# Optimization experiments

Measured on AMD Instinct MI355X. Metric: run time of the kernel, lower is better.

## Reference

```python
import jax, jax.numpy as jnp
import numpy as np


def _rgcn(x, src, dst, et, basis, comp, root, bias):
    # Basis-decomposed RGCNConv (PyG semantics): per-relation mean aggregation
    # over incoming edges + root transform + bias.
    N = x.shape[0]
    R = comp.shape[0]
    W = jnp.einsum('rb,bio->rio', comp, basis)          # [R, in, out]
    xr = jnp.einsum('ni,rio->rno', x, W)                 # [R, N, out]
    msg = xr[et, src]                                    # [E, out] gather per edge
    seg = dst * R + et                                   # (target, relation) segment id
    cnt = jax.ops.segment_sum(jnp.ones(et.shape, x.dtype), seg, num_segments=N * R)
    norm = 1.0 / jnp.maximum(cnt, 1.0)                   # mean per (dst, relation)
    msg = msg * norm[seg][:, None]
    agg = jax.ops.segment_sum(msg, dst, num_segments=N)  # scatter-add to targets
    return agg + x @ root + bias


def setup_inputs() -> dict:
    key = jax.random.key(0)
    ks = jax.random.split(key, 20)
    N, E, R, B, F, D, C, NB = 100000, 1600000, 5, 512, 4, 32, 5, 2
    s = 0.1
    inp = {
        'x': jax.random.normal(ks[0], (N, F), jnp.float32),
        'edge_index': jax.random.randint(ks[1], (2, E), 0, N, dtype=jnp.int32),
        'edge_type': jax.random.randint(ks[2], (E,), 0, R, dtype=jnp.int32),
        'start_nodes': jax.random.randint(ks[3], (B,), 0, N, dtype=jnp.int32),
        # layer 0: in=F, out=D
        'basis0': jax.random.normal(ks[4], (NB, F, D), jnp.float32) * s,
        'comp0': jax.random.normal(ks[5], (R, NB), jnp.float32) * s,
        'root0': jax.random.normal(ks[6], (F, D), jnp.float32) * s,
        'bias0': jax.random.normal(ks[7], (D,), jnp.float32) * s,
        # layers 1..3: in=out=D, stacked
        'basis': jax.random.normal(ks[8], (3, NB, D, D), jnp.float32) * s,
        'comp': jax.random.normal(ks[9], (3, R, NB), jnp.float32) * s,
        'root': jax.random.normal(ks[10], (3, D, D), jnp.float32) * s,
        'bias': jax.random.normal(ks[11], (3, D), jnp.float32) * s,
        # MLP head: sum(latent_dim)=128 -> 128 -> C
        'lin1_w': jax.random.normal(ks[12], (4 * D, 128), jnp.float32) * s,
        'lin1_b': jax.random.normal(ks[13], (128,), jnp.float32) * s,
        'lin2_w': jax.random.normal(ks[14], (128, C), jnp.float32) * s,
        'lin2_b': jax.random.normal(ks[15], (C,), jnp.float32) * s,
    }
    return inp


def reference(x, edge_index, edge_type, start_nodes, basis0, comp0, root0, bias0,
              basis, comp, root, bias, lin1_w, lin1_b, lin2_w, lin2_b):
    src, dst = edge_index[0], edge_index[1]
    h = jnp.tanh(_rgcn(x, src, dst, edge_type, basis0, comp0, root0, bias0))
    states = [h]
    for l in range(basis.shape[0]):
        h = jnp.tanh(_rgcn(h, src, dst, edge_type, basis[l], comp[l], root[l], bias[l]))
        states.append(h)
    concat = jnp.concatenate(states, axis=1)             # [N, 128]
    # Per-graph readout: the walk's degenerate n_walks=1 branch, i.e. the
    # start (user) node's concatenated state (sequential backtracking walk
    # replaced by its deterministic initialization path; eval mode, no dropout).
    acc = concat[start_nodes]                            # [B, 128]
    h1 = jax.nn.relu(acc @ lin1_w + lin1_b)
    logits = h1 @ lin2_w + lin2_b
    return jax.nn.log_softmax(logits, axis=-1)
```

## Files before the change

### kernel.cpp

```cpp
#include <hip/hip_runtime.h>
#include <cstdint>

#define N_NODES 100000
#define N_EDGES 1600000
#define R_REL   5
#define NBASIS  2
#define B_START 512
#define PART_SZ 12500
#define NBUCK   256
#define BUCK_SZ 391
#define EPB     6250
#define STAGE_CAP 7000

__device__ __forceinline__ unsigned short f2bf(float f) {
    unsigned u = __float_as_uint(f);
    unsigned r = (u + 0x7FFF + ((u >> 16) & 1)) >> 16;
    return (unsigned short)r;
}


__global__ __launch_bounds__(256) void k_cntb(
    const int* __restrict__ ei, int* __restrict__ bhist) {
    __shared__ int lh[NBUCK];
    int tid = threadIdx.x;
    lh[tid] = 0;
    __syncthreads();
    int base = blockIdx.x * EPB;
    for (int j = tid; j < EPB; j += 256) {
        int dst = ei[N_EDGES + base + j];
        atomicAdd(&lh[dst / BUCK_SZ], 1);
    }
    __syncthreads();
    bhist[blockIdx.x * NBUCK + tid] = lh[tid];
}

__global__ __launch_bounds__(256) void k_scanb(
    int* __restrict__ bhist, int* __restrict__ bbase) {
    int b = threadIdx.x;
    int tot = 0;
    for (int i = 0; i < NBUCK; i += 8) {
        int v0 = bhist[(i + 0) * NBUCK + b], v1 = bhist[(i + 1) * NBUCK + b];
        int v2 = bhist[(i + 2) * NBUCK + b], v3 = bhist[(i + 3) * NBUCK + b];
        int v4 = bhist[(i + 4) * NBUCK + b], v5 = bhist[(i + 5) * NBUCK + b];
        int v6 = bhist[(i + 6) * NBUCK + b], v7 = bhist[(i + 7) * NBUCK + b];
        tot += v0 + v1 + v2 + v3 + v4 + v5 + v6 + v7;
    }
    __shared__ int s[NBUCK];
    s[b] = tot;
    __syncthreads();
    for (int o = 1; o < NBUCK; o <<= 1) {
        int v = (b >= o) ? s[b - o] : 0;
        __syncthreads();
        s[b] += v;
        __syncthreads();
    }
    int base = s[b] - tot;
    bbase[b] = base;
    if (b == NBUCK - 1) bbase[NBUCK] = s[NBUCK - 1];
    int run = base;
    for (int i = 0; i < NBUCK; i += 8) {
        int v0 = bhist[(i + 0) * NBUCK + b], v1 = bhist[(i + 1) * NBUCK + b];
        int v2 = bhist[(i + 2) * NBUCK + b], v3 = bhist[(i + 3) * NBUCK + b];
        int v4 = bhist[(i + 4) * NBUCK + b], v5 = bhist[(i + 5) * NBUCK + b];
        int v6 = bhist[(i + 6) * NBUCK + b], v7 = bhist[(i + 7) * NBUCK + b];
        bhist[(i + 0) * NBUCK + b] = run; run += v0;
        bhist[(i + 1) * NBUCK + b] = run; run += v1;
        bhist[(i + 2) * NBUCK + b] = run; run += v2;
        bhist[(i + 3) * NBUCK + b] = run; run += v3;
        bhist[(i + 4) * NBUCK + b] = run; run += v4;
        bhist[(i + 5) * NBUCK + b] = run; run += v5;
        bhist[(i + 6) * NBUCK + b] = run; run += v6;
        bhist[(i + 7) * NBUCK + b] = run; run += v7;
    }
}

__global__ __launch_bounds__(256) void k_scat(
    const int* __restrict__ ei, const int* __restrict__ et,
    const int* __restrict__ bhist, int* __restrict__ arena) {
    __shared__ int lc[NBUCK];
    int tid = threadIdx.x;
    lc[tid] = bhist[blockIdx.x * NBUCK + tid];
    __syncthreads();
    int base = blockIdx.x * EPB;
    for (int j = tid; j < EPB; j += 256) {
        int e   = base + j;
        int src = ei[e];
        int dst = ei[N_EDGES + e];
        int t   = et[e];
        int bk  = dst / BUCK_SZ;
        int dl  = dst - bk * BUCK_SZ;
        int pos = atomicAdd(&lc[bk], 1);
        arena[pos] = src | (t << 17) | (dl << 20);
    }
}

__global__ __launch_bounds__(256) void k_build(
    const int* __restrict__ arena, const int* __restrict__ bbase,
    int* __restrict__ off, int* __restrict__ pk_m, float* __restrict__ pk_nv) {
    __shared__ int deg5[BUCK_SZ * R_REL];
    __shared__ int loff[BUCK_SZ + 1];
    __shared__ int cur[BUCK_SZ];
    __shared__ int stg[STAGE_CAP];
    int b = blockIdx.x, tid = threadIdx.x;
    int base = bbase[b], end = bbase[b + 1];
    int count = end - base;
    for (int i = tid; i < BUCK_SZ * R_REL; i += 256) deg5[i] = 0;
    __syncthreads();
    for (int i = tid; i < count; i += 256) {
        int r  = arena[base + i];
        int dl = ((unsigned)r) >> 20;
        int t  = (r >> 17) & 7;
        atomicAdd(&deg5[dl * R_REL + t], 1);
    }
    __syncthreads();
    if (tid == 0) {
        int run = 0;
        for (int dl = 0; dl < BUCK_SZ; dl++) {
            loff[dl] = run;
            run += deg5[dl * R_REL + 0] + deg5[dl * R_REL + 1] +
                   deg5[dl * R_REL + 2] + deg5[dl * R_REL + 3] +
                   deg5[dl * R_REL + 4];
        }
        loff[BUCK_SZ] = run;
    }
    __syncthreads();
    for (int dl = tid; dl < BUCK_SZ; dl += 256) {
        int n = b * BUCK_SZ + dl;
        if (n < N_NODES) off[n] = base + loff[dl];
        cur[dl] = loff[dl];
    }
    if (b == NBUCK - 1 && tid == 0) off[N_NODES] = N_EDGES;
    __syncthreads();
    for (int i = tid; i < count; i += 256) {
        int r  = arena[base + i];
        int dl = ((unsigned)r) >> 20;
        int rk = atomicAdd(&cur[dl], 1);
        if (rk < STAGE_CAP) stg[rk] = r;
    }
    __syncthreads();
    for (int i = tid; i < count; i += 256) {
        int r   = stg[i < STAGE_CAP ? i : STAGE_CAP - 1];
        int src = r & 0x1FFFF;
        int t   = (r >> 17) & 7;
        int dl  = ((unsigned)r) >> 20;
        int c   = deg5[dl * R_REL + t];
        pk_m[base + i]  = src | (t << 20);
        pk_nv[base + i] = 1.0f / (float)(c > 0 ? c : 1);
    }
}


template <int IN>
__global__ __launch_bounds__(256) void k_xform(
    const float* __restrict__ h_in, float* __restrict__ h_io,
    unsigned short* __restrict__ y5, const float* __restrict__ basis,
    const float* __restrict__ root, const float* __restrict__ biasL,
    const float* __restrict__ compL) {
    int tid  = threadIdx.x;
    int lane = tid & 31;
    int sub  = tid >> 5;
    int g    = blockIdx.x * 8 + sub;
    float w0[IN], w1[IN], wr[IN];
#pragma unroll
    for (int i = 0; i < IN; i++) {
        w0[i] = basis[i * 32 + lane];
        w1[i] = basis[IN * 32 + i * 32 + lane];
        wr[i] = root[i * 32 + lane];
    }
    float c0[R_REL], c1[R_REL];
#pragma unroll
    for (int r = 0; r < R_REL; r++) {
        c0[r] = compL[r * NBASIS + 0];
        c1[r] = compL[r * NBASIS + 1];
    }
    float bv = biasL[lane];
    for (int n = g; n < N_NODES; n += 8192) {
        float hn = (lane < IN) ? h_in[n * IN + lane] : 0.f;
        float a0 = 0.f, a1 = 0.f, ar = bv;
#pragma unroll
        for (int i = 0; i < IN; i++) {
            float v = __shfl(hn, i, 32);
            a0 += v * w0[i];
            a1 += v * w1[i];
            ar += v * wr[i];
        }
#pragma unroll
        for (int r = 0; r < R_REL; r++)
            y5[(size_t)r * N_NODES * 32 + n * 32 + lane] = f2bf(c0[r] * a0 + c1[r] * a1);
        h_io[n * 32 + lane] = ar;
    }
}


__global__ __launch_bounds__(256) void k_edge(
    const unsigned short* __restrict__ y5, float* __restrict__ h,
    const int* __restrict__ pk_m, const float* __restrict__ pk_nv,
    const int* __restrict__ off) {
    int tid  = threadIdx.x;
    int lane = tid & 31;
    int sub  = tid >> 5;
    int part  = blockIdx.x & 7;
    int local = (blockIdx.x >> 3) * 8 + sub;
    if (local >= PART_SZ) return;
    int n = part * PART_SZ + local;

    float acc = h[n * 32 + lane];
    int e0 = off[n], e1 = off[n + 1];
    for (int base = e0; base < e1; base += 32) {
        int idx = base + lane;
        bool vld = idx < e1;
        int   m  = vld ? pk_m[idx] : 0;
        float nv = vld ? pk_nv[idx] : 0.f;
        int kmax = e1 - base;
        if (kmax > 32) kmax = 32;
        int kk = (kmax + 7) & ~7;
        for (int j = 0; j < kk; j += 8) {
            int m0 = __shfl(m, j + 0, 32), m1 = __shfl(m, j + 1, 32);
            int m2 = __shfl(m, j + 2, 32), m3 = __shfl(m, j + 3, 32);
            int m4 = __shfl(m, j + 4, 32), m5 = __shfl(m, j + 5, 32);
            int m6 = __shfl(m, j + 6, 32), m7 = __shfl(m, j + 7, 32);
            unsigned r0 = ((unsigned)m0 >> 20) * N_NODES + (m0 & 0xFFFFF);
            unsigned r1 = ((unsigned)m1 >> 20) * N_NODES + (m1 & 0xFFFFF);
            unsigned r2 = ((unsigned)m2 >> 20) * N_NODES + (m2 & 0xFFFFF);
            unsigned r3 = ((unsigned)m3 >> 20) * N_NODES + (m3 & 0xFFFFF);
            unsigned r4 = ((unsigned)m4 >> 20) * N_NODES + (m4 & 0xFFFFF);
            unsigned r5 = ((unsigned)m5 >> 20) * N_NODES + (m5 & 0xFFFFF);
            unsigned r6 = ((unsigned)m6 >> 20) * N_NODES + (m6 & 0xFFFFF);
            unsigned r7 = ((unsigned)m7 >> 20) * N_NODES + (m7 & 0xFFFFF);
            unsigned short u0 = y5[(size_t)r0 * 32 + lane];
            unsigned short u1 = y5[(size_t)r1 * 32 + lane];
            unsigned short u2 = y5[(size_t)r2 * 32 + lane];
            unsigned short u3 = y5[(size_t)r3 * 32 + lane];
            unsigned short u4 = y5[(size_t)r4 * 32 + lane];
            unsigned short u5 = y5[(size_t)r5 * 32 + lane];
            unsigned short u6 = y5[(size_t)r6 * 32 + lane];
            unsigned short u7 = y5[(size_t)r7 * 32 + lane];
            float v0 = __shfl(nv, j + 0, 32), v1 = __shfl(nv, j + 1, 32);
            float v2 = __shfl(nv, j + 2, 32), v3 = __shfl(nv, j + 3, 32);
            float v4 = __shfl(nv, j + 4, 32), v5 = __shfl(nv, j + 5, 32);
            float v6 = __shfl(nv, j + 6, 32), v7 = __shfl(nv, j + 7, 32);
            acc += v0 * __uint_as_float((unsigned)u0 << 16);
            acc += v1 * __uint_as_float((unsigned)u1 << 16);
            acc += v2 * __uint_as_float((unsigned)u2 << 16);
            acc += v3 * __uint_as_float((unsigned)u3 << 16);
            acc += v4 * __uint_as_float((unsigned)u4 << 16);
            acc += v5 * __uint_as_float((unsigned)u5 << 16);
            acc += v6 * __uint_as_float((unsigned)u6 << 16);
            acc += v7 * __uint_as_float((unsigned)u7 << 16);
        }
    }
    h[n * 32 + lane] = tanhf(acc);
}


__global__ void k_save(const float* __restrict__ h, const int* __restrict__ start,
                       float* __restrict__ sav) {
    int t = blockIdx.x * blockDim.x + threadIdx.x;
    if (t < B_START * 32) {
        int b = t >> 5, ln = t & 31;
        sav[t] = h[start[b] * 32 + ln];
    }
}

__global__ __launch_bounds__(128) void k_mlp(
    const float* __restrict__ sav, const float* __restrict__ w1,
    const float* __restrict__ b1, const float* __restrict__ w2,
    const float* __restrict__ b2, float* __restrict__ out) {
    __shared__ float cvec[128];
    __shared__ float hb[128];
    __shared__ float lg[8];
    int b = blockIdx.x, t = threadIdx.x;
    cvec[t] = sav[(t >> 5) * (B_START * 32) + b * 32 + (t & 31)];
    __syncthreads();
    float a = b1[t];
#pragma unroll 8
    for (int k = 0; k < 128; k++) a += cvec[k] * w1[k * 128 + t];
    hb[t] = fmaxf(a, 0.f);
    __syncthreads();
    if (t < 5) {
        float a2 = b2[t];
        for (int k = 0; k < 128; k++) a2 += hb[k] * w2[k * 5 + t];
        lg[t] = a2;
    }
    __syncthreads();
    if (t < 5) {
        float m = lg[0];
        for (int j = 1; j < 5; j++) m = fmaxf(m, lg[j]);
        float s = 0.f;
        for (int j = 0; j < 5; j++) s += expf(lg[j] - m);
        out[b * 5 + t] = lg[t] - m - logf(s);
    }
}


extern "C" void kernel_launch(void* const* d_in, const int* in_sizes, int n_in,
                              void* d_out, int out_size, void* d_ws, size_t ws_size,
                              hipStream_t stream) {
    const float* x      = (const float*)d_in[0];
    const int*   ei     = (const int*)d_in[1];
    const int*   etype  = (const int*)d_in[2];
    const int*   start  = (const int*)d_in[3];
    const float* basis0 = (const float*)d_in[4];
    const float* comp0  = (const float*)d_in[5];
    const float* root0  = (const float*)d_in[6];
    const float* bias0  = (const float*)d_in[7];
    const float* basis  = (const float*)d_in[8];
    const float* comp   = (const float*)d_in[9];
    const float* root   = (const float*)d_in[10];
    const float* bias   = (const float*)d_in[11];
    const float* w1     = (const float*)d_in[12];
    const float* b1     = (const float*)d_in[13];
    const float* w2     = (const float*)d_in[14];
    const float* b2     = (const float*)d_in[15];
    float* out = (float*)d_out;

    char* p = (char*)d_ws;
    auto alloc = [&](size_t bytes) -> void* {
        void* r = (void*)p;
        p += (bytes + 255) & ~(size_t)255;
        return r;
    };
    int*            off   = (int*)alloc((N_NODES + 1) * 4);
    int*            bhist = (int*)alloc((size_t)NBUCK * NBUCK * 4);
    int*            bbase = (int*)alloc((NBUCK + 1) * 4);
    int*            arena = (int*)alloc((size_t)N_EDGES * 4);
    int*            pk_m  = (int*)alloc((size_t)N_EDGES * 4);
    float*          pk_nv = (float*)alloc((size_t)N_EDGES * 4);
    float*          h     = (float*)alloc((size_t)N_NODES * 32 * 4);
    unsigned short* y5    = (unsigned short*)alloc((size_t)R_REL * N_NODES * 32 * 2);
    float*          sav   = (float*)alloc(4 * B_START * 32 * 4);

    k_cntb<<<NBUCK, 256, 0, stream>>>(ei, bhist);
    k_scanb<<<1, 256, 0, stream>>>(bhist, bbase);
    k_scat<<<NBUCK, 256, 0, stream>>>(ei, etype, bhist, arena);
    k_build<<<NBUCK, 256, 0, stream>>>(arena, bbase, off, pk_m, pk_nv);

    int nbEdge = 8 * ((PART_SZ + 7) / 8);
    k_xform<4><<<1024, 256, 0, stream>>>(x, h, y5, basis0, root0, bias0, comp0);
    k_edge<<<nbEdge, 256, 0, stream>>>(y5, h, pk_m, pk_nv, off);
    k_save<<<64, 256, 0, stream>>>(h, start, sav);
    for (int l = 0; l < 3; l++) {
        k_xform<32><<<1024, 256, 0, stream>>>(h, h, y5,
                                              basis + (size_t)l * 2048,
                                              root + (size_t)l * 1024,
                                              bias + l * 32,
                                              comp + l * 10);
        k_edge<<<nbEdge, 256, 0, stream>>>(y5, h, pk_m, pk_nv, off);
        k_save<<<64, 256, 0, stream>>>(h, start, sav + (l + 1) * 16384);
    }

    k_mlp<<<B_START, 128, 0, stream>>>(sav, w1, b1, w2, b2, out);
}
```

Baseline: 402.2 us.

## Switch edge aggregation to edge-parallel runs with segmented atomic flushes

Replaces the per-destination-node CSR loop in the edge kernel with fixed 32-edge runs per wavefront half. Each run does a segmented reduction over the dst-sorted edges and flushes partial sums with atomicAdd into h. This removes load imbalance and the tail loop overhead of variable-degree nodes. Because h is now accumulated atomically, tanh moves into the next transform's input load, the save kernel is fused into that transform, and ping-pong h buffers are used. The cost is extra atomics at node boundaries and a new per-edge destination array.

```diff
diff --git a/kernel.cpp b/kernel.cpp
--- a/kernel.cpp
+++ b/kernel.cpp
@@ -6,7 +6,6 @@
 #define R_REL   5
 #define NBASIS  2
 #define B_START 512
-#define PART_SZ 12500
 #define NBUCK   256
 #define BUCK_SZ 391
 #define EPB     6250
@@ -96,7 +95,8 @@
 
 __global__ __launch_bounds__(256) void k_build(
     const int* __restrict__ arena, const int* __restrict__ bbase,
-    int* __restrict__ off, int* __restrict__ pk_m, float* __restrict__ pk_nv) {
+    int* __restrict__ pk_m, float* __restrict__ pk_nv,
+    int* __restrict__ pk_dst) {
     __shared__ int deg5[BUCK_SZ * R_REL];
     __shared__ int loff[BUCK_SZ + 1];
     __shared__ int cur[BUCK_SZ];
@@ -124,12 +124,7 @@
         loff[BUCK_SZ] = run;
     }
     __syncthreads();
-    for (int dl = tid; dl < BUCK_SZ; dl += 256) {
-        int n = b * BUCK_SZ + dl;
-        if (n < N_NODES) off[n] = base + loff[dl];
-        cur[dl] = loff[dl];
-    }
-    if (b == NBUCK - 1 && tid == 0) off[N_NODES] = N_EDGES;
+    for (int dl = tid; dl < BUCK_SZ; dl += 256) cur[dl] = loff[dl];
     __syncthreads();
     for (int i = tid; i < count; i += 256) {
         int r  = arena[base + i];
@@ -144,22 +139,28 @@
         int t   = (r >> 17) & 7;
         int dl  = ((unsigned)r) >> 20;
         int c   = deg5[dl * R_REL + t];
-        pk_m[base + i]  = src | (t << 20);
-        pk_nv[base + i] = 1.0f / (float)(c > 0 ? c : 1);
-    }
-}
-
-
-template <int IN>
+        pk_m[base + i]   = src | (t << 17);
+        pk_nv[base + i]  = 1.0f / (float)(c > 0 ? c : 1);
+        pk_dst[base + i] = b * BUCK_SZ + dl;
+    }
+}
+
+
+template <int IN, bool TIN>
 __global__ __launch_bounds__(256) void k_xform(
-    const float* __restrict__ h_in, float* __restrict__ h_io,
+    const float* __restrict__ h_in, float* __restrict__ h_out,
     unsigned short* __restrict__ y5, const float* __restrict__ basis,
     const float* __restrict__ root, const float* __restrict__ biasL,
-    const float* __restrict__ compL) {
+    const float* __restrict__ compL, const int* __restrict__ start,
+    float* __restrict__ sav) {
     int tid  = threadIdx.x;
     int lane = tid & 31;
     int sub  = tid >> 5;
     int g    = blockIdx.x * 8 + sub;
+    if (IN == 32 && sav != nullptr && g < B_START) {
+        int row = start[g];
+        sav[g * 32 + lane] = tanhf(h_in[row * 32 + lane]);
+    }
     float w0[IN], w1[IN], wr[IN];
 #pragma unroll
     for (int i = 0; i < IN; i++) {
@@ -176,6 +177,7 @@
     float bv = biasL[lane];
     for (int n = g; n < N_NODES; n += 8192) {
         float hn = (lane < IN) ? h_in[n * IN + lane] : 0.f;
+        if (TIN) hn = tanhf(hn);
         float a0 = 0.f, a1 = 0.f, ar = bv;
 #pragma unroll
         for (int i = 0; i < IN; i++) {
@@ -187,7 +189,7 @@
 #pragma unroll
         for (int r = 0; r < R_REL; r++)
             y5[(size_t)r * N_NODES * 32 + n * 32 + lane] = f2bf(c0[r] * a0 + c1[r] * a1);
-        h_io[n * 32 + lane] = ar;
+        h_out[n * 32 + lane] = ar;
     }
 }
 
@@ -195,70 +197,57 @@
 __global__ __launch_bounds__(256) void k_edge(
     const unsigned short* __restrict__ y5, float* __restrict__ h,
     const int* __restrict__ pk_m, const float* __restrict__ pk_nv,
-    const int* __restrict__ off) {
+    const int* __restrict__ pk_dst) {
     int tid  = threadIdx.x;
     int lane = tid & 31;
     int sub  = tid >> 5;
-    int part  = blockIdx.x & 7;
-    int local = (blockIdx.x >> 3) * 8 + sub;
-    if (local >= PART_SZ) return;
-    int n = part * PART_SZ + local;
-
-    float acc = h[n * 32 + lane];
-    int e0 = off[n], e1 = off[n + 1];
-    for (int base = e0; base < e1; base += 32) {
-        int idx = base + lane;
-        bool vld = idx < e1;
-        int   m  = vld ? pk_m[idx] : 0;
-        float nv = vld ? pk_nv[idx] : 0.f;
-        int kmax = e1 - base;
-        if (kmax > 32) kmax = 32;
-        int kk = (kmax + 7) & ~7;
-        for (int j = 0; j < kk; j += 8) {
-            int m0 = __shfl(m, j + 0, 32), m1 = __shfl(m, j + 1, 32);
-            int m2 = __shfl(m, j + 2, 32), m3 = __shfl(m, j + 3, 32);
-            int m4 = __shfl(m, j + 4, 32), m5 = __shfl(m, j + 5, 32);
-            int m6 = __shfl(m, j + 6, 32), m7 = __shfl(m, j + 7, 32);
-            unsigned r0 = ((unsigned)m0 >> 20) * N_NODES + (m0 & 0xFFFFF);
-            unsigned r1 = ((unsigned)m1 >> 20) * N_NODES + (m1 & 0xFFFFF);
-            unsigned r2 = ((unsigned)m2 >> 20) * N_NODES + (m2 & 0xFFFFF);
-            unsigned r3 = ((unsigned)m3 >> 20) * N_NODES + (m3 & 0xFFFFF);
-            unsigned r4 = ((unsigned)m4 >> 20) * N_NODES + (m4 & 0xFFFFF);
-            unsigned r5 = ((unsigned)m5 >> 20) * N_NODES + (m5 & 0xFFFFF);
-            unsigned r6 = ((unsigned)m6 >> 20) * N_NODES + (m6 & 0xFFFFF);
-            unsigned r7 = ((unsigned)m7 >> 20) * N_NODES + (m7 & 0xFFFFF);
-            unsigned short u0 = y5[(size_t)r0 * 32 + lane];
-            unsigned short u1 = y5[(size_t)r1 * 32 + lane];
-            unsigned short u2 = y5[(size_t)r2 * 32 + lane];
-            unsigned short u3 = y5[(size_t)r3 * 32 + lane];
-            unsigned short u4 = y5[(size_t)r4 * 32 + lane];
-            unsigned short u5 = y5[(size_t)r5 * 32 + lane];
-            unsigned short u6 = y5[(size_t)r6 * 32 + lane];
-            unsigned short u7 = y5[(size_t)r7 * 32 + lane];
-            float v0 = __shfl(nv, j + 0, 32), v1 = __shfl(nv, j + 1, 32);
-            float v2 = __shfl(nv, j + 2, 32), v3 = __shfl(nv, j + 3, 32);
-            float v4 = __shfl(nv, j + 4, 32), v5 = __shfl(nv, j + 5, 32);
-            float v6 = __shfl(nv, j + 6, 32), v7 = __shfl(nv, j + 7, 32);
-            acc += v0 * __uint_as_float((unsigned)u0 << 16);
-            acc += v1 * __uint_as_float((unsigned)u1 << 16);
-            acc += v2 * __uint_as_float((unsigned)u2 << 16);
-            acc += v3 * __uint_as_float((unsigned)u3 << 16);
-            acc += v4 * __uint_as_float((unsigned)u4 << 16);
-            acc += v5 * __uint_as_float((unsigned)u5 << 16);
-            acc += v6 * __uint_as_float((unsigned)u6 << 16);
-            acc += v7 * __uint_as_float((unsigned)u7 << 16);
+    int run  = blockIdx.x * 8 + sub;
+    int base = run * 32;
+    if (base >= N_EDGES) return;
+    int idx = base + lane;
+    int   m  = pk_m[idx];
+    float nv = pk_nv[idx];
+    int   d  = pk_dst[idx];
+
+    float acc = 0.f;
+    int dcur = __shfl(d, 0, 32);
+#pragma unroll
+    for (int j = 0; j < 32; j += 8) {
+        int mm[8];
+#pragma unroll
+        for (int q = 0; q < 8; q++) mm[q] = __shfl(m, j + q, 32);
+        unsigned short uu[8];
+#pragma unroll
+        for (int q = 0; q < 8; q++) {
+            unsigned r = ((unsigned)mm[q] >> 17) * N_NODES + (mm[q] & 0x1FFFF);
+            uu[q] = y5[(size_t)r * 32 + lane];
         }
-    }
-    h[n * 32 + lane] = tanhf(acc);
-}
-
-
-__global__ void k_save(const float* __restrict__ h, const int* __restrict__ start,
-                       float* __restrict__ sav) {
+        float val[8];
+#pragma unroll
+        for (int q = 0; q < 8; q++)
+            val[q] = __shfl(nv, j + q, 32) *
+                     __uint_as_float((unsigned)uu[q] << 16);
+#pragma unroll
+        for (int q = 0; q < 8; q++) {
+            int dj = __shfl(d, j + q, 32);
+            if (dj != dcur) {
+                atomicAdd(&h[(size_t)dcur * 32 + lane], acc);
+                acc = 0.f;
+                dcur = dj;
+            }
+            acc += val[q];
+        }
+    }
+    atomicAdd(&h[(size_t)dcur * 32 + lane], acc);
+}
+
+
+__global__ void k_saveT(const float* __restrict__ h, const int* __restrict__ start,
+                        float* __restrict__ sav) {
     int t = blockIdx.x * blockDim.x + threadIdx.x;
     if (t < B_START * 32) {
         int b = t >> 5, ln = t & 31;
-        sav[t] = h[start[b] * 32 + ln];
+        sav[t] = tanhf(h[start[b] * 32 + ln]);
     }
 }
 
@@ -320,34 +309,36 @@
         p += (bytes + 255) & ~(size_t)255;
         return r;
     };
-    int*            off   = (int*)alloc((N_NODES + 1) * 4);
-    int*            bhist = (int*)alloc((size_t)NBUCK * NBUCK * 4);
-    int*            bbase = (int*)alloc((NBUCK + 1) * 4);
-    int*            arena = (int*)alloc((size_t)N_EDGES * 4);
-    int*            pk_m  = (int*)alloc((size_t)N_EDGES * 4);
-    float*          pk_nv = (float*)alloc((size_t)N_EDGES * 4);
-    float*          h     = (float*)alloc((size_t)N_NODES * 32 * 4);
-    unsigned short* y5    = (unsigned short*)alloc((size_t)R_REL * N_NODES * 32 * 2);
-    float*          sav   = (float*)alloc(4 * B_START * 32 * 4);
+    int*            bhist  = (int*)alloc((size_t)NBUCK * NBUCK * 4);
+    int*            bbase  = (int*)alloc((NBUCK + 1) * 4);
+    int*            arena  = (int*)alloc((size_t)N_EDGES * 4);
+    int*            pk_m   = (int*)alloc((size_t)N_EDGES * 4);
+    float*          pk_nv  = (float*)alloc((size_t)N_EDGES * 4);
+    int*            pk_dst = (int*)alloc((size_t)N_EDGES * 4);
+    float*          hA     = (float*)alloc((size_t)N_NODES * 32 * 4);
+    float*          hB     = (float*)alloc((size_t)N_NODES * 32 * 4);
+    unsigned short* y5     = (unsigned short*)alloc((size_t)R_REL * N_NODES * 32 * 2);
+    float*          sav    = (float*)alloc(4 * B_START * 32 * 4);
 
     k_cntb<<<NBUCK, 256, 0, stream>>>(ei, bhist);
     k_scanb<<<1, 256, 0, stream>>>(bhist, bbase);
     k_scat<<<NBUCK, 256, 0, stream>>>(ei, etype, bhist, arena);
-    k_build<<<NBUCK, 256, 0, stream>>>(arena, bbase, off, pk_m, pk_nv);
-
-    int nbEdge = 8 * ((PART_SZ + 7) / 8);
-    k_xform<4><<<1024, 256, 0, stream>>>(x, h, y5, basis0, root0, bias0, comp0);
-    k_edge<<<nbEdge, 256, 0, stream>>>(y5, h, pk_m, pk_nv, off);
-    k_save<<<64, 256, 0, stream>>>(h, start, sav);
+    k_build<<<NBUCK, 256, 0, stream>>>(arena, bbase, pk_m, pk_nv, pk_dst);
+
+    int nbEdge = (N_EDGES / 32 + 7) / 8;
+    k_xform<4, false><<<1024, 256, 0, stream>>>(x, hA, y5, basis0, root0,
+                                                bias0, comp0, start, nullptr);
+    k_edge<<<nbEdge, 256, 0, stream>>>(y5, hA, pk_m, pk_nv, pk_dst);
+    float* hin = hA;
+    float* hout = hB;
     for (int l = 0; l < 3; l++) {
-        k_xform<32><<<1024, 256, 0, stream>>>(h, h, y5,
-                                              basis + (size_t)l * 2048,
-                                              root + (size_t)l * 1024,
-                                              bias + l * 32,
-                                              comp + l * 10);
-        k_edge<<<nbEdge, 256, 0, stream>>>(y5, h, pk_m, pk_nv, off);
-        k_save<<<64, 256, 0, stream>>>(h, start, sav + (l + 1) * 16384);
-    }
+        k_xform<32, true><<<1024, 256, 0, stream>>>(
+            hin, hout, y5, basis + (size_t)l * 2048, root + (size_t)l * 1024,
+            bias + l * 32, comp + l * 10, start, sav + l * 16384);
+        k_edge<<<nbEdge, 256, 0, stream>>>(y5, hout, pk_m, pk_nv, pk_dst);
+        float* tmp = hin; hin = hout; hout = tmp;
+    }
+    k_saveT<<<64, 256, 0, stream>>>(hin, start, sav + 3 * 16384);
 
     k_mlp<<<B_START, 128, 0, stream>>>(sav, w1, b1, w2, b2, out);
 }
```

New measurement: 411.5 us. +2.3%, slower.

## Split edge aggregation into source-sorted message gather and dst-ordered accumulation

Applied to the files above, without the earlier changes.

Adds a second bucket sort of edges by (source,relation) key and interleaves the per-node relation outputs so each source's five relation rows are contiguous. A new message kernel gathers 64-byte rows with int4 loads in source order, scales them by the mean norm, and writes bf16 messages to a dst-ordered buffer. An accumulation kernel then streams those messages contiguously per destination. The aim is to swap scattered 2-byte gathers for more coalesced, cache-local reads. In exchange it adds a 100 MB message buffer write and read per layer, three extra preprocessing kernels, and rounds each scaled message to bf16.

```diff
diff --git a/kernel.cpp b/kernel.cpp
--- a/kernel.cpp
+++ b/kernel.cpp
@@ -9,6 +9,7 @@
 #define PART_SZ 12500
 #define NBUCK   256
 #define BUCK_SZ 391
+#define KB_SZ   1954
 #define EPB     6250
 #define STAGE_CAP 7000
 
@@ -16,6 +17,12 @@
     unsigned u = __float_as_uint(f);
     unsigned r = (u + 0x7FFF + ((u >> 16) & 1)) >> 16;
     return (unsigned short)r;
+}
+
+__device__ __forceinline__ int pack2(int u, float nv) {
+    float a = __uint_as_float(((unsigned)u) << 16) * nv;
+    float b = __uint_as_float((unsigned)u & 0xFFFF0000u) * nv;
+    return (int)f2bf(a) | ((int)f2bf(b) << 16);
 }
 
 
@@ -144,16 +151,53 @@
         int t   = (r >> 17) & 7;
         int dl  = ((unsigned)r) >> 20;
         int c   = deg5[dl * R_REL + t];
-        pk_m[base + i]  = src | (t << 20);
+        pk_m[base + i]  = src | (t << 17);
         pk_nv[base + i] = 1.0f / (float)(c > 0 ? c : 1);
+    }
+}
+
+
+__global__ __launch_bounds__(256) void k_cnt2(
+    const int* __restrict__ pk_m, int* __restrict__ bhist2) {
+    __shared__ int lh[NBUCK];
+    int tid = threadIdx.x;
+    lh[tid] = 0;
+    __syncthreads();
+    int base = blockIdx.x * EPB;
+    for (int j = tid; j < EPB; j += 256) {
+        int m = pk_m[base + j];
+        int key = (m & 0x1FFFF) * R_REL + ((m >> 17) & 7);
+        atomicAdd(&lh[key / KB_SZ], 1);
+    }
+    __syncthreads();
+    bhist2[blockIdx.x * NBUCK + tid] = lh[tid];
+}
+
+__global__ __launch_bounds__(256) void k_scat2(
+    const int* __restrict__ pk_m, const float* __restrict__ pk_nv,
+    const int* __restrict__ bhist2, int* __restrict__ se_m,
+    float* __restrict__ se_nv, int* __restrict__ se_slot) {
+    __shared__ int lc[NBUCK];
+    int tid = threadIdx.x;
+    lc[tid] = bhist2[blockIdx.x * NBUCK + tid];
+    __syncthreads();
+    int base = blockIdx.x * EPB;
+    for (int j = tid; j < EPB; j += 256) {
+        int i = base + j;
+        int m = pk_m[i];
+        int key = (m & 0x1FFFF) * R_REL + ((m >> 17) & 7);
+        int pos = atomicAdd(&lc[key / KB_SZ], 1);
+        se_m[pos]    = m;
+        se_nv[pos]   = pk_nv[i];
+        se_slot[pos] = i;
     }
 }
 
 
 template <int IN>
 __global__ __launch_bounds__(256) void k_xform(
-    const float* __restrict__ h_in, float* __restrict__ h_io,
-    unsigned short* __restrict__ y5, const float* __restrict__ basis,
+    const float* __restrict__ h_in, float* __restrict__ hbase,
+    unsigned short* __restrict__ ySE, const float* __restrict__ basis,
     const float* __restrict__ root, const float* __restrict__ biasL,
     const float* __restrict__ compL) {
     int tid  = threadIdx.x;
@@ -186,68 +230,67 @@
         }
 #pragma unroll
         for (int r = 0; r < R_REL; r++)
-            y5[(size_t)r * N_NODES * 32 + n * 32 + lane] = f2bf(c0[r] * a0 + c1[r] * a1);
-        h_io[n * 32 + lane] = ar;
-    }
-}
-
-
-__global__ __launch_bounds__(256) void k_edge(
-    const unsigned short* __restrict__ y5, float* __restrict__ h,
-    const int* __restrict__ pk_m, const float* __restrict__ pk_nv,
-    const int* __restrict__ off) {
-    int tid  = threadIdx.x;
-    int lane = tid & 31;
-    int sub  = tid >> 5;
+            ySE[(size_t)n * (R_REL * 32) + r * 32 + lane] =
+                f2bf(c0[r] * a0 + c1[r] * a1);
+        hbase[n * 32 + lane] = ar;
+    }
+}
+
+
+__global__ __launch_bounds__(256) void k_msg(
+    const unsigned short* __restrict__ ySE, const int* __restrict__ se_m,
+    const float* __restrict__ se_nv, const int* __restrict__ se_slot,
+    unsigned short* __restrict__ msgb) {
+    int p = blockIdx.x & 7, q = blockIdx.x >> 3;
+    int L = p * 782 + q;
+    if (L >= N_EDGES / 256) return;
+    int tid = threadIdx.x;
+    int wv = tid >> 6, ln = tid & 63;
+    int idx = L * 256 + wv * 64 + ln;
+    int   mL  = se_m[idx];
+    float nvL = se_nv[idx];
+    int   sL  = se_slot[idx];
+    int team = ln >> 2, tl = ln & 3;
+    const int4* __restrict__ y4 = (const int4*)ySE;
+    int4* __restrict__ mb4 = (int4*)msgb;
+#pragma unroll
+    for (int r = 0; r < 4; r++) {
+        int e = r * 16 + team;
+        int m      = __shfl(mL, e, 64);
+        float nv   = __shfl(nvL, e, 64);
+        int slot   = __shfl(sL, e, 64);
+        unsigned key = (unsigned)(m & 0x1FFFF) * R_REL + (unsigned)((m >> 17) & 7);
+        int4 v = y4[(size_t)key * 4 + tl];
+        int4 o;
+        o.x = pack2(v.x, nv);
+        o.y = pack2(v.y, nv);
+        o.z = pack2(v.z, nv);
+        o.w = pack2(v.w, nv);
+        mb4[(size_t)slot * 4 + tl] = o;
+    }
+}
+
+
+__global__ __launch_bounds__(256) void k_acc(
+    const float* __restrict__ hbase, float* __restrict__ h,
+    const unsigned short* __restrict__ msgb, const int* __restrict__ off) {
+    int tid = threadIdx.x, lane = tid & 31, sub = tid >> 5;
     int part  = blockIdx.x & 7;
     int local = (blockIdx.x >> 3) * 8 + sub;
     if (local >= PART_SZ) return;
     int n = part * PART_SZ + local;
-
-    float acc = h[n * 32 + lane];
+    float acc = hbase[n * 32 + lane];
     int e0 = off[n], e1 = off[n + 1];
-    for (int base = e0; base < e1; base += 32) {
-        int idx = base + lane;
-        bool vld = idx < e1;
-        int   m  = vld ? pk_m[idx] : 0;
-        float nv = vld ? pk_nv[idx] : 0.f;
-        int kmax = e1 - base;
-        if (kmax > 32) kmax = 32;
-        int kk = (kmax + 7) & ~7;
-        for (int j = 0; j < kk; j += 8) {
-            int m0 = __shfl(m, j + 0, 32), m1 = __shfl(m, j + 1, 32);
-            int m2 = __shfl(m, j + 2, 32), m3 = __shfl(m, j + 3, 32);
-            int m4 = __shfl(m, j + 4, 32), m5 = __shfl(m, j + 5, 32);
-            int m6 = __shfl(m, j + 6, 32), m7 = __shfl(m, j + 7, 32);
-            unsigned r0 = ((unsigned)m0 >> 20) * N_NODES + (m0 & 0xFFFFF);
-            unsigned r1 = ((unsigned)m1 >> 20) * N_NODES + (m1 & 0xFFFFF);
-            unsigned r2 = ((unsigned)m2 >> 20) * N_NODES + (m2 & 0xFFFFF);
-            unsigned r3 = ((unsigned)m3 >> 20) * N_NODES + (m3 & 0xFFFFF);
-            unsigned r4 = ((unsigned)m4 >> 20) * N_NODES + (m4 & 0xFFFFF);
-            unsigned r5 = ((unsigned)m5 >> 20) * N_NODES + (m5 & 0xFFFFF);
-            unsigned r6 = ((unsigned)m6 >> 20) * N_NODES + (m6 & 0xFFFFF);
-            unsigned r7 = ((unsigned)m7 >> 20) * N_NODES + (m7 & 0xFFFFF);
-            unsigned short u0 = y5[(size_t)r0 * 32 + lane];
-            unsigned short u1 = y5[(size_t)r1 * 32 + lane];
-            unsigned short u2 = y5[(size_t)r2 * 32 + lane];
-            unsigned short u3 = y5[(size_t)r3 * 32 + lane];
-            unsigned short u4 = y5[(size_t)r4 * 32 + lane];
-            unsigned short u5 = y5[(size_t)r5 * 32 + lane];
-            unsigned short u6 = y5[(size_t)r6 * 32 + lane];
-            unsigned short u7 = y5[(size_t)r7 * 32 + lane];
-            float v0 = __shfl(nv, j + 0, 32), v1 = __shfl(nv, j + 1, 32);
-            float v2 = __shfl(nv, j + 2, 32), v3 = __shfl(nv, j + 3, 32);
-            float v4 = __shfl(nv, j + 4, 32), v5 = __shfl(nv, j + 5, 32);
-            float v6 = __shfl(nv, j + 6, 32), v7 = __shfl(nv, j + 7, 32);
-            acc += v0 * __uint_as_float((unsigned)u0 << 16);
-            acc += v1 * __uint_as_float((unsigned)u1 << 16);
-            acc += v2 * __uint_as_float((unsigned)u2 << 16);
-            acc += v3 * __uint_as_float((unsigned)u3 << 16);
-            acc += v4 * __uint_as_float((unsigned)u4 << 16);
-            acc += v5 * __uint_as_float((unsigned)u5 << 16);
-            acc += v6 * __uint_as_float((unsigned)u6 << 16);
-            acc += v7 * __uint_as_float((unsigned)u7 << 16);
+    for (int base = e0; base < e1; base += 8) {
+        float s = 0.f;
+#pragma unroll
+        for (int q = 0; q < 8; q++) {
+            int e = base + q;
+            unsigned short u = (e < e1) ? msgb[(size_t)e * 32 + lane]
+                                        : (unsigned short)0;
+            s += __uint_as_float((unsigned)u << 16);
         }
+        acc += s;
     }
     h[n * 32 + lane] = tanhf(acc);
 }
@@ -320,32 +363,45 @@
         p += (bytes + 255) & ~(size_t)255;
         return r;
     };
-    int*            off   = (int*)alloc((N_NODES + 1) * 4);
-    int*            bhist = (int*)alloc((size_t)NBUCK * NBUCK * 4);
-    int*            bbase = (int*)alloc((NBUCK + 1) * 4);
-    int*            arena = (int*)alloc((size_t)N_EDGES * 4);
-    int*            pk_m  = (int*)alloc((size_t)N_EDGES * 4);
-    float*          pk_nv = (float*)alloc((size_t)N_EDGES * 4);
-    float*          h     = (float*)alloc((size_t)N_NODES * 32 * 4);
-    unsigned short* y5    = (unsigned short*)alloc((size_t)R_REL * N_NODES * 32 * 2);
-    float*          sav   = (float*)alloc(4 * B_START * 32 * 4);
+    int*            bhist   = (int*)alloc((size_t)NBUCK * NBUCK * 4);
+    int*            bbase   = (int*)alloc((NBUCK + 1) * 4);
+    int*            bhist2  = (int*)alloc((size_t)NBUCK * NBUCK * 4);
+    int*            bbase2  = (int*)alloc((NBUCK + 1) * 4);
+    int*            arena   = (int*)alloc((size_t)N_EDGES * 4);
+    int*            off     = (int*)alloc((N_NODES + 1) * 4);
+    int*            pk_m    = (int*)alloc((size_t)N_EDGES * 4);
+    float*          pk_nv   = (float*)alloc((size_t)N_EDGES * 4);
+    int*            se_m    = (int*)alloc((size_t)N_EDGES * 4);
+    float*          se_nv   = (float*)alloc((size_t)N_EDGES * 4);
+    int*            se_slot = (int*)alloc((size_t)N_EDGES * 4);
+    float*          hbase   = (float*)alloc((size_t)N_NODES * 32 * 4);
+    float*          h       = (float*)alloc((size_t)N_NODES * 32 * 4);
+    unsigned short* ySE     = (unsigned short*)alloc((size_t)N_NODES * R_REL * 32 * 2);
+    unsigned short* msgb    = (unsigned short*)alloc((size_t)N_EDGES * 32 * 2);
+    float*          sav     = (float*)alloc(4 * B_START * 32 * 4);
 
     k_cntb<<<NBUCK, 256, 0, stream>>>(ei, bhist);
     k_scanb<<<1, 256, 0, stream>>>(bhist, bbase);
     k_scat<<<NBUCK, 256, 0, stream>>>(ei, etype, bhist, arena);
     k_build<<<NBUCK, 256, 0, stream>>>(arena, bbase, off, pk_m, pk_nv);
-
-    int nbEdge = 8 * ((PART_SZ + 7) / 8);
-    k_xform<4><<<1024, 256, 0, stream>>>(x, h, y5, basis0, root0, bias0, comp0);
-    k_edge<<<nbEdge, 256, 0, stream>>>(y5, h, pk_m, pk_nv, off);
+    k_cnt2<<<NBUCK, 256, 0, stream>>>(pk_m, bhist2);
+    k_scanb<<<1, 256, 0, stream>>>(bhist2, bbase2);
+    k_scat2<<<NBUCK, 256, 0, stream>>>(pk_m, pk_nv, bhist2, se_m, se_nv, se_slot);
+
+    int nbMsg = 8 * 782;
+    int nbAcc = 8 * ((PART_SZ + 7) / 8);
+    k_xform<4><<<1024, 256, 0, stream>>>(x, hbase, ySE, basis0, root0, bias0, comp0);
+    k_msg<<<nbMsg, 256, 0, stream>>>(ySE, se_m, se_nv, se_slot, msgb);
+    k_acc<<<nbAcc, 256, 0, stream>>>(hbase, h, msgb, off);
     k_save<<<64, 256, 0, stream>>>(h, start, sav);
     for (int l = 0; l < 3; l++) {
-        k_xform<32><<<1024, 256, 0, stream>>>(h, h, y5,
+        k_xform<32><<<1024, 256, 0, stream>>>(h, hbase, ySE,
                                               basis + (size_t)l * 2048,
                                               root + (size_t)l * 1024,
                                               bias + l * 32,
                                               comp + l * 10);
-        k_edge<<<nbEdge, 256, 0, stream>>>(y5, h, pk_m, pk_nv, off);
+        k_msg<<<nbMsg, 256, 0, stream>>>(ySE, se_m, se_nv, se_slot, msgb);
+        k_acc<<<nbAcc, 256, 0, stream>>>(hbase, h, msgb, off);
         k_save<<<64, 256, 0, stream>>>(h, start, sav + (l + 1) * 16384);
     }
 
```

New measurement: 619.0 us. +53.9%, slower.

## Gather per-node int8 basis projections and apply relation coefficients per edge

Applied to the files above, without the earlier changes.

The transform kernel no longer writes five bf16 relation-specific projections per node. It stores the two basis projections as int8 pairs packed into one 16-bit word, plus one scale per node. The edge kernel gathers this single packed table indexed by source only, and folds the per-relation comp coefficients, the node scale and the mean normalisation into two per-edge factors. This shrinks the gather table fivefold and removes the relation offset from the addressing. The cost is int8 quantisation error, an extra per-edge load of the scale, and a second FMA per edge.

```diff
diff --git a/kernel.cpp b/kernel.cpp
--- a/kernel.cpp
+++ b/kernel.cpp
@@ -11,12 +11,6 @@
 #define BUCK_SZ 391
 #define EPB     6250
 #define STAGE_CAP 7000
-
-__device__ __forceinline__ unsigned short f2bf(float f) {
-    unsigned u = __float_as_uint(f);
-    unsigned r = (u + 0x7FFF + ((u >> 16) & 1)) >> 16;
-    return (unsigned short)r;
-}
 
 
 __global__ __launch_bounds__(256) void k_cntb(
@@ -144,7 +138,7 @@
         int t   = (r >> 17) & 7;
         int dl  = ((unsigned)r) >> 20;
         int c   = deg5[dl * R_REL + t];
-        pk_m[base + i]  = src | (t << 20);
+        pk_m[base + i]  = src | (t << 17);
         pk_nv[base + i] = 1.0f / (float)(c > 0 ? c : 1);
     }
 }
@@ -153,9 +147,10 @@
 template <int IN>
 __global__ __launch_bounds__(256) void k_xform(
     const float* __restrict__ h_in, float* __restrict__ h_io,
-    unsigned short* __restrict__ y5, const float* __restrict__ basis,
-    const float* __restrict__ root, const float* __restrict__ biasL,
-    const float* __restrict__ compL) {
+    unsigned short* __restrict__ ypk, float* __restrict__ sc,
+    const float* __restrict__ basis, const float* __restrict__ root,
+    const float* __restrict__ biasL, const float* __restrict__ compL) {
+    (void)compL;
     int tid  = threadIdx.x;
     int lane = tid & 31;
     int sub  = tid >> 5;
@@ -166,12 +161,6 @@
         w0[i] = basis[i * 32 + lane];
         w1[i] = basis[IN * 32 + i * 32 + lane];
         wr[i] = root[i * 32 + lane];
-    }
-    float c0[R_REL], c1[R_REL];
-#pragma unroll
-    for (int r = 0; r < R_REL; r++) {
-        c0[r] = compL[r * NBASIS + 0];
-        c1[r] = compL[r * NBASIS + 1];
     }
     float bv = biasL[lane];
     for (int n = g; n < N_NODES; n += 8192) {
@@ -184,19 +173,29 @@
             a1 += v * w1[i];
             ar += v * wr[i];
         }
+        float mx = fmaxf(fabsf(a0), fabsf(a1));
 #pragma unroll
-        for (int r = 0; r < R_REL; r++)
-            y5[(size_t)r * N_NODES * 32 + n * 32 + lane] = f2bf(c0[r] * a0 + c1[r] * a1);
+        for (int k = 16; k >= 1; k >>= 1)
+            mx = fmaxf(mx, __shfl_xor(mx, k, 32));
+        float inv = (mx > 0.f) ? 127.0f / mx : 0.f;
+        int q0 = __float2int_rn(a0 * inv);
+        int q1 = __float2int_rn(a1 * inv);
+        ypk[n * 32 + lane] = (unsigned short)((q0 & 0xFF) | ((q1 & 0xFF) << 8));
+        if (lane == 0) sc[n] = mx * (1.0f / 127.0f);
         h_io[n * 32 + lane] = ar;
     }
 }
 
 
 __global__ __launch_bounds__(256) void k_edge(
-    const unsigned short* __restrict__ y5, float* __restrict__ h,
-    const int* __restrict__ pk_m, const float* __restrict__ pk_nv,
-    const int* __restrict__ off) {
-    int tid  = threadIdx.x;
+    const unsigned short* __restrict__ ypk, const float* __restrict__ sc,
+    float* __restrict__ h, const int* __restrict__ pk_m,
+    const float* __restrict__ pk_nv, const int* __restrict__ off,
+    const float* __restrict__ compL) {
+    __shared__ float Cl[2 * R_REL];
+    int tid = threadIdx.x;
+    if (tid < 2 * R_REL) Cl[tid] = compL[tid];
+    __syncthreads();
     int lane = tid & 31;
     int sub  = tid >> 5;
     int part  = blockIdx.x & 7;
@@ -211,6 +210,11 @@
         bool vld = idx < e1;
         int   m  = vld ? pk_m[idx] : 0;
         float nv = vld ? pk_nv[idx] : 0.f;
+        int srcL = m & 0x1FFFF;
+        int etL  = (m >> 17) & 7;
+        float sv = sc[srcL] * nv;
+        float cc0 = sv * Cl[etL * 2];
+        float cc1 = sv * Cl[etL * 2 + 1];
         int kmax = e1 - base;
         if (kmax > 32) kmax = 32;
         int kk = (kmax + 7) & ~7;
@@ -219,34 +223,38 @@
             int m2 = __shfl(m, j + 2, 32), m3 = __shfl(m, j + 3, 32);
             int m4 = __shfl(m, j + 4, 32), m5 = __shfl(m, j + 5, 32);
             int m6 = __shfl(m, j + 6, 32), m7 = __shfl(m, j + 7, 32);
-            unsigned r0 = ((unsigned)m0 >> 20) * N_NODES + (m0 & 0xFFFFF);
-            unsigned r1 = ((unsigned)m1 >> 20) * N_NODES + (m1 & 0xFFFFF);
-            unsigned r2 = ((unsigned)m2 >> 20) * N_NODES + (m2 & 0xFFFFF);
-            unsigned r3 = ((unsigned)m3 >> 20) * N_NODES + (m3 & 0xFFFFF);
-            unsigned r4 = ((unsigned)m4 >> 20) * N_NODES + (m4 & 0xFFFFF);
-            unsigned r5 = ((unsigned)m5 >> 20) * N_NODES + (m5 & 0xFFFFF);
-            unsigned r6 = ((unsigned)m6 >> 20) * N_NODES + (m6 & 0xFFFFF);
-            unsigned r7 = ((unsigned)m7 >> 20) * N_NODES + (m7 & 0xFFFFF);
-            unsigned short u0 = y5[(size_t)r0 * 32 + lane];
-            unsigned short u1 = y5[(size_t)r1 * 32 + lane];
-            unsigned short u2 = y5[(size_t)r2 * 32 + lane];
-            unsigned short u3 = y5[(size_t)r3 * 32 + lane];
-            unsigned short u4 = y5[(size_t)r4 * 32 + lane];
-            unsigned short u5 = y5[(size_t)r5 * 32 + lane];
-            unsigned short u6 = y5[(size_t)r6 * 32 + lane];
-            unsigned short u7 = y5[(size_t)r7 * 32 + lane];
-            float v0 = __shfl(nv, j + 0, 32), v1 = __shfl(nv, j + 1, 32);
-            float v2 = __shfl(nv, j + 2, 32), v3 = __shfl(nv, j + 3, 32);
-            float v4 = __shfl(nv, j + 4, 32), v5 = __shfl(nv, j + 5, 32);
-            float v6 = __shfl(nv, j + 6, 32), v7 = __shfl(nv, j + 7, 32);
-            acc += v0 * __uint_as_float((unsigned)u0 << 16);
-            acc += v1 * __uint_as_float((unsigned)u1 << 16);
-            acc += v2 * __uint_as_float((unsigned)u2 << 16);
-            acc += v3 * __uint_as_float((unsigned)u3 << 16);
-            acc += v4 * __uint_as_float((unsigned)u4 << 16);
-            acc += v5 * __uint_as_float((unsigned)u5 << 16);
-            acc += v6 * __uint_as_float((unsigned)u6 << 16);
-            acc += v7 * __uint_as_float((unsigned)u7 << 16);
+            unsigned short u0 = ypk[(size_t)(m0 & 0x1FFFF) * 32 + lane];
+            unsigned short u1 = ypk[(size_t)(m1 & 0x1FFFF) * 32 + lane];
+            unsigned short u2 = ypk[(size_t)(m2 & 0x1FFFF) * 32 + lane];
+            unsigned short u3 = ypk[(size_t)(m3 & 0x1FFFF) * 32 + lane];
+            unsigned short u4 = ypk[(size_t)(m4 & 0x1FFFF) * 32 + lane];
+            unsigned short u5 = ypk[(size_t)(m5 & 0x1FFFF) * 32 + lane];
+            unsigned short u6 = ypk[(size_t)(m6 & 0x1FFFF) * 32 + lane];
+            unsigned short u7 = ypk[(size_t)(m7 & 0x1FFFF) * 32 + lane];
+            float x0 = __shfl(cc0, j + 0, 32), z0 = __shfl(cc1, j + 0, 32);
+            float x1 = __shfl(cc0, j + 1, 32), z1 = __shfl(cc1, j + 1, 32);
+            float x2 = __shfl(cc0, j + 2, 32), z2 = __shfl(cc1, j + 2, 32);
+            float x3 = __shfl(cc0, j + 3, 32), z3 = __shfl(cc1, j + 3, 32);
+            float x4 = __shfl(cc0, j + 4, 32), z4 = __shfl(cc1, j + 4, 32);
+            float x5 = __shfl(cc0, j + 5, 32), z5 = __shfl(cc1, j + 5, 32);
+            float x6 = __shfl(cc0, j + 6, 32), z6 = __shfl(cc1, j + 6, 32);
+            float x7 = __shfl(cc0, j + 7, 32), z7 = __shfl(cc1, j + 7, 32);
+            acc += x0 * (float)(int)(signed char)(u0 & 0xFF)
+                 + z0 * (float)(int)(signed char)(u0 >> 8);
+            acc += x1 * (float)(int)(signed char)(u1 & 0xFF)
+                 + z1 * (float)(int)(signed char)(u1 >> 8);
+            acc += x2 * (float)(int)(signed char)(u2 & 0xFF)
+                 + z2 * (float)(int)(signed char)(u2 >> 8);
+            acc += x3 * (float)(int)(signed char)(u3 & 0xFF)
+                 + z3 * (float)(int)(signed char)(u3 >> 8);
+            acc += x4 * (float)(int)(signed char)(u4 & 0xFF)
+                 + z4 * (float)(int)(signed char)(u4 >> 8);
+            acc += x5 * (float)(int)(signed char)(u5 & 0xFF)
+                 + z5 * (float)(int)(signed char)(u5 >> 8);
+            acc += x6 * (float)(int)(signed char)(u6 & 0xFF)
+                 + z6 * (float)(int)(signed char)(u6 >> 8);
+            acc += x7 * (float)(int)(signed char)(u7 & 0xFF)
+                 + z7 * (float)(int)(signed char)(u7 >> 8);
         }
     }
     h[n * 32 + lane] = tanhf(acc);
@@ -320,14 +328,15 @@
         p += (bytes + 255) & ~(size_t)255;
         return r;
     };
-    int*            off   = (int*)alloc((N_NODES + 1) * 4);
     int*            bhist = (int*)alloc((size_t)NBUCK * NBUCK * 4);
     int*            bbase = (int*)alloc((NBUCK + 1) * 4);
     int*            arena = (int*)alloc((size_t)N_EDGES * 4);
+    int*            off   = (int*)alloc((N_NODES + 1) * 4);
     int*            pk_m  = (int*)alloc((size_t)N_EDGES * 4);
     float*          pk_nv = (float*)alloc((size_t)N_EDGES * 4);
+    unsigned short* ypk   = (unsigned short*)alloc((size_t)N_NODES * 32 * 2);
+    float*          sc    = (float*)alloc((size_t)N_NODES * 4);
     float*          h     = (float*)alloc((size_t)N_NODES * 32 * 4);
-    unsigned short* y5    = (unsigned short*)alloc((size_t)R_REL * N_NODES * 32 * 2);
     float*          sav   = (float*)alloc(4 * B_START * 32 * 4);
 
     k_cntb<<<NBUCK, 256, 0, stream>>>(ei, bhist);
@@ -336,16 +345,17 @@
     k_build<<<NBUCK, 256, 0, stream>>>(arena, bbase, off, pk_m, pk_nv);
 
     int nbEdge = 8 * ((PART_SZ + 7) / 8);
-    k_xform<4><<<1024, 256, 0, stream>>>(x, h, y5, basis0, root0, bias0, comp0);
-    k_edge<<<nbEdge, 256, 0, stream>>>(y5, h, pk_m, pk_nv, off);
+    k_xform<4><<<1024, 256, 0, stream>>>(x, h, ypk, sc, basis0, root0, bias0, comp0);
+    k_edge<<<nbEdge, 256, 0, stream>>>(ypk, sc, h, pk_m, pk_nv, off, comp0);
     k_save<<<64, 256, 0, stream>>>(h, start, sav);
     for (int l = 0; l < 3; l++) {
-        k_xform<32><<<1024, 256, 0, stream>>>(h, h, y5,
+        k_xform<32><<<1024, 256, 0, stream>>>(h, h, ypk, sc,
                                               basis + (size_t)l * 2048,
                                               root + (size_t)l * 1024,
                                               bias + l * 32,
                                               comp + l * 10);
-        k_edge<<<nbEdge, 256, 0, stream>>>(y5, h, pk_m, pk_nv, off);
+        k_edge<<<nbEdge, 256, 0, stream>>>(ypk, sc, h, pk_m, pk_nv, off,
+                                           comp + l * 10);
         k_save<<<64, 256, 0, stream>>>(h, start, sav + (l + 1) * 16384);
     }
 
```

After: 443.4 us. +10.3%, slower.
